# Kernel tuning notes

Hardware: AMD Instinct MI355X
Metric: run time of the kernel (lower is better)

The kernel has to match this reference:

```python
import jax, jax.numpy as jnp
import numpy as np

N_NODES = 100000
N_EDGES = 800000
HID = 128
LN_EPS = 1e-5


def _mlp2(x, w1, b1, w2, b2):
    # Linear -> ReLU -> Linear
    return jax.nn.relu(x @ w1 + b1) @ w2 + b2


def setup_inputs() -> dict:
    key = jax.random.key(0)
    ks = jax.random.split(key, 12)
    s = 1.0 / np.sqrt(3 * HID)
    s2 = 1.0 / np.sqrt(HID)
    return {
        "h": jax.random.normal(ks[0], (N_NODES, HID), dtype=jnp.float32),
        "edge_index": jax.random.randint(ks[1], (2, N_EDGES), 0, N_NODES, dtype=jnp.int64),
        "edge_x": jax.random.normal(ks[2], (N_EDGES, HID), dtype=jnp.float32),
        # edge_proj MLP (weights stored [in, out])
        "ep_w1": jax.random.uniform(ks[3], (3 * HID, HID), jnp.float32, -s, s),
        "ep_b1": jax.random.uniform(ks[4], (HID,), jnp.float32, -s, s),
        "ep_w2": jax.random.uniform(ks[5], (HID, HID), jnp.float32, -s2, s2),
        "ep_b2": jax.random.uniform(ks[6], (HID,), jnp.float32, -s2, s2),
        # update MLP
        "up_w1": jax.random.uniform(ks[7], (3 * HID, HID), jnp.float32, -s, s),
        "up_b1": jax.random.uniform(ks[8], (HID,), jnp.float32, -s, s),
        "up_w2": jax.random.uniform(ks[9], (HID, HID), jnp.float32, -s2, s2),
        "up_b2": jax.random.uniform(ks[10], (HID,), jnp.float32, -s2, s2),
        # LayerNorm affine
        "ln_g": jnp.ones((HID,), jnp.float32),
        "ln_b": jnp.zeros((HID,), jnp.float32),
    }


def reference(h, edge_index, edge_x, ep_w1, ep_b1, ep_w2, ep_b2,
              up_w1, up_b1, up_w2, up_b2, ln_g, ln_b):
    n = h.shape[0]
    src, dst = edge_index[0], edge_index[1]
    # edge gather + concat -> [E, 3H] -> message MLP -> [E, H]
    messages = _mlp2(jnp.concatenate([h[src], h[dst], edge_x], axis=-1),
                     ep_w1, ep_b1, ep_w2, ep_b2)
    # scatter-add aggregation for both directions
    incoming = jax.ops.segment_sum(messages, dst, num_segments=n)
    outgoing = jax.ops.segment_sum(messages, src, num_segments=n)
    # degree normalization (clamp min 1)
    ones = jnp.ones((edge_index.shape[1],), h.dtype)
    in_deg = jnp.maximum(jax.ops.segment_sum(ones, dst, num_segments=n), 1.0)[:, None]
    out_deg = jnp.maximum(jax.ops.segment_sum(ones, src, num_segments=n), 1.0)[:, None]
    updated = _mlp2(jnp.concatenate([h, incoming / in_deg, outgoing / out_deg], axis=-1),
                    up_w1, up_b1, up_w2, up_b2)
    # residual + LayerNorm
    x = h + updated
    mu = jnp.mean(x, axis=-1, keepdims=True)
    var = jnp.mean(jnp.square(x - mu), axis=-1, keepdims=True)
    return (x - mu) * jax.lax.rsqrt(var + LN_EPS) * ln_g + ln_b
```

## Files before the change

kernel.cpp:

```cpp
#include <hip/hip_runtime.h>
#include <stdint.h>

#define HIDD 128
#define NNODES 100000
#define NEDGES 800000

typedef short s16x8 __attribute__((ext_vector_type(8)));
typedef float f32x4 __attribute__((ext_vector_type(4)));

__device__ __forceinline__ short f2bf(float f) {
  union { float f; unsigned u; } v; v.f = f;
  return (short)((v.u + 0x7fffu + ((v.u >> 16) & 1u)) >> 16);
}
__device__ __forceinline__ short4 cvt4(float4 v) {
  short4 s; s.x = f2bf(v.x); s.y = f2bf(v.y); s.z = f2bf(v.z); s.w = f2bf(v.w);
  return s;
}
__device__ __forceinline__ float bflo(unsigned w) {
  union { unsigned u; float f; } v; v.u = w << 16; return v.f;
}
__device__ __forceinline__ float bfhi(unsigned w) {
  union { unsigned u; float f; } v; v.u = w & 0xffff0000u; return v.f;
}
__device__ __forceinline__ unsigned pack2(float a, float b) {
  return ((unsigned)(unsigned short)f2bf(b) << 16) | (unsigned)(unsigned short)f2bf(a);
}
__device__ __forceinline__ f32x4 mfma16(s16x8 a, s16x8 b, f32x4 c) {
  return __builtin_amdgcn_mfma_f32_16x16x32_bf16(a, b, c, 0, 0, 0);
}
__device__ __forceinline__ void atomic_pk_bf16(unsigned short* addr, unsigned pk) {
  asm volatile("global_atomic_pk_add_bf16 %0, %1, off" :: "v"(addr), "v"(pk) : "memory");
}

__global__ void k_prep_h(const float4* __restrict__ h4, short4* __restrict__ hb4, int n4) {
  int stride = gridDim.x * blockDim.x;
  for (int i = blockIdx.x * blockDim.x + threadIdx.x; i < n4; i += stride)
    hb4[i] = cvt4(h4[i]);
}

__global__ void k_prep_w(const float* __restrict__ w1e, const float* __restrict__ w2e,
                         const float* __restrict__ w1u, const float* __restrict__ w2u,
                         short* __restrict__ w1et, short* __restrict__ w2et,
                         short* __restrict__ w1ut, short* __restrict__ w2ut) {
  int i = blockIdx.x * 256 + threadIdx.x;
  if (i < 49152) {
    int n = i / 384, k = i - n * 384;
    w1et[i] = f2bf(w1e[k * 128 + n]);
    w1ut[i] = f2bf(w1u[k * 128 + n]);
  } else {
    int j = i - 49152;
    if (j < 16384) {
      int n = j >> 7, k = j & 127;
      int oc = (n & ~31) + 2 * (n & 15) + ((n >> 4) & 1);
      w2et[j] = f2bf(w2e[k * 128 + oc]);
      w2ut[j] = f2bf(w2u[k * 128 + n]);
    }
  }
}

__global__ __launch_bounds__(256, 2)
void k_edge(const short* __restrict__ hb, const int* __restrict__ eidx,
            const float* __restrict__ ex,
            const short* __restrict__ w1t, const short* __restrict__ w2t,
            const float* __restrict__ b1g, const float* __restrict__ b2g,
            unsigned short* __restrict__ incb, unsigned short* __restrict__ outgb,
            float* __restrict__ indeg, float* __restrict__ outdeg) {
  __shared__ __align__(16) short Xs[64][392];
  __shared__ __align__(16) short Hs[64][136];

  const int tid = threadIdx.x;
  const int wave = tid >> 6, lane = tid & 63;
  const int lg = lane >> 4, lr = lane & 15;
  const int koff = lg * 8;
  const int c0 = wave * 32 + lr, c1 = c0 + 16;
  const int pc0 = wave * 32 + 2 * lr;

  s16x8 wb1a[12], wb1b[12], wb2a[4], wb2b[4];
#pragma unroll
  for (int kk = 0; kk < 12; ++kk) {
    wb1a[kk] = *(const s16x8*)(w1t + c0 * 384 + kk * 32 + koff);
    wb1b[kk] = *(const s16x8*)(w1t + c1 * 384 + kk * 32 + koff);
  }
#pragma unroll
  for (int kk = 0; kk < 4; ++kk) {
    wb2a[kk] = *(const s16x8*)(w2t + c0 * 128 + kk * 32 + koff);
    wb2b[kk] = *(const s16x8*)(w2t + c1 * 128 + kk * 32 + koff);
  }
  const float bias1_0 = b1g[c0], bias1_1 = b1g[c1];
  const float bias2_0 = b2g[pc0], bias2_1 = b2g[pc0 + 1];

  for (int t = blockIdx.x; t < NEDGES / 64; t += gridDim.x) {
    const int base = t * 64;

    for (int u = tid; u < 64 * 32; u += 256) {
      int r = u >> 5, c = u & 31;
      int node = (c < 16) ? eidx[base + r] : eidx[NEDGES + base + r];
      *(int4*)&Xs[r][c * 8] = *(const int4*)(hb + (long)node * 128 + (c & 15) * 8);
    }
    for (int u = tid; u < 64 * 32; u += 256) {
      int r = u >> 5, q = u & 31;
      float4 v = *(const float4*)(ex + (long)(base + r) * 128 + q * 4);
      *(short4*)&Xs[r][256 + q * 4] = cvt4(v);
    }
    if (tid < 64) {
      atomicAdd(&outdeg[eidx[base + tid]], 1.0f);
      atomicAdd(&indeg[eidx[NEDGES + base + tid]], 1.0f);
    }
    __syncthreads();

    f32x4 acc[4][2] = {};
#pragma unroll
    for (int kk = 0; kk < 12; ++kk) {
      int k0 = kk * 32 + koff;
#pragma unroll
      for (int m = 0; m < 4; ++m) {
        s16x8 a = *(const s16x8*)&Xs[m * 16 + lr][k0];
        acc[m][0] = mfma16(a, wb1a[kk], acc[m][0]);
        acc[m][1] = mfma16(a, wb1b[kk], acc[m][1]);
      }
    }
#pragma unroll
    for (int m = 0; m < 4; ++m)
#pragma unroll
      for (int r2 = 0; r2 < 4; ++r2) {
        int row = m * 16 + lg * 4 + r2;
        Hs[row][c0] = f2bf(fmaxf(acc[m][0][r2] + bias1_0, 0.f));
        Hs[row][c1] = f2bf(fmaxf(acc[m][1][r2] + bias1_1, 0.f));
      }
    __syncthreads();

    f32x4 acc2[4][2] = {};
#pragma unroll
    for (int kk = 0; kk < 4; ++kk) {
      int k0 = kk * 32 + koff;
#pragma unroll
      for (int m = 0; m < 4; ++m) {
        s16x8 a = *(const s16x8*)&Hs[m * 16 + lr][k0];
        acc2[m][0] = mfma16(a, wb2a[kk], acc2[m][0]);
        acc2[m][1] = mfma16(a, wb2b[kk], acc2[m][1]);
      }
    }
#pragma unroll
    for (int m = 0; m < 4; ++m)
#pragma unroll
      for (int r2 = 0; r2 < 4; ++r2) {
        int row = m * 16 + lg * 4 + r2;
        int s = eidx[base + row], d = eidx[NEDGES + base + row];
        unsigned pk = pack2(acc2[m][0][r2] + bias2_0, acc2[m][1][r2] + bias2_1);
        atomic_pk_bf16(outgb + (long)s * 128 + pc0, pk);
        atomic_pk_bf16(incb + (long)d * 128 + pc0, pk);
      }
  }
}

__global__ __launch_bounds__(256, 2)
void k_node(const float* __restrict__ h, const short* __restrict__ hb,
            const unsigned short* __restrict__ incb,
            const unsigned short* __restrict__ outgb,
            const float* __restrict__ indeg, const float* __restrict__ outdeg,
            const short* __restrict__ w1t, const short* __restrict__ w2t,
            const float* __restrict__ b1g, const float* __restrict__ b2g,
            const float* __restrict__ lng, const float* __restrict__ lnb,
            float* __restrict__ out) {
  __shared__ __align__(16) char smem[67584];
  short (*Xs)[392] = (short (*)[392])smem;
  float (*Xf)[132] = (float (*)[132])smem;
  short (*Hs)[136] = (short (*)[136])(smem + 50176);

  const int tid = threadIdx.x;
  const int wave = tid >> 6, lane = tid & 63;
  const int lg = lane >> 4, lr = lane & 15;
  const int koff = lg * 8;
  const int c0 = wave * 32 + lr, c1 = c0 + 16;

  s16x8 wb1a[12], wb1b[12], wb2a[4], wb2b[4];
#pragma unroll
  for (int kk = 0; kk < 12; ++kk) {
    wb1a[kk] = *(const s16x8*)(w1t + c0 * 384 + kk * 32 + koff);
    wb1b[kk] = *(const s16x8*)(w1t + c1 * 384 + kk * 32 + koff);
  }
#pragma unroll
  for (int kk = 0; kk < 4; ++kk) {
    wb2a[kk] = *(const s16x8*)(w2t + c0 * 128 + kk * 32 + koff);
    wb2b[kk] = *(const s16x8*)(w2t + c1 * 128 + kk * 32 + koff);
  }
  const float bias1_0 = b1g[c0], bias1_1 = b1g[c1];
  const float bias2_0 = b2g[c0], bias2_1 = b2g[c1];

  const int ntiles = (NNODES + 63) / 64;
  for (int t = blockIdx.x; t < ntiles; t += gridDim.x) {
    const int base = t * 64;

    for (int u = tid; u < 64 * 16; u += 256) {
      int r = u >> 4, c = u & 15;
      long node = min(base + r, NNODES - 1);
      *(int4*)&Xs[r][c * 8] = *(const int4*)(hb + node * 128 + c * 8);
    }
    for (int u = tid; u < 64 * 16; u += 256) {
      int r = u >> 4, c = u & 15;
      long node = min(base + r, NNODES - 1);
      float s = 1.f / fmaxf(indeg[node], 1.f);
      uint4 w = *(const uint4*)(incb + node * 128 + c * 8);
      unsigned o0 = pack2(bflo(w.x) * s, bfhi(w.x) * s);
      unsigned o1 = pack2(bflo(w.y) * s, bfhi(w.y) * s);
      unsigned o2 = pack2(bflo(w.z) * s, bfhi(w.z) * s);
      unsigned o3 = pack2(bflo(w.w) * s, bfhi(w.w) * s);
      *(uint4*)&Xs[r][128 + c * 8] = make_uint4(o0, o1, o2, o3);
    }
    for (int u = tid; u < 64 * 16; u += 256) {
      int r = u >> 4, c = u & 15;
      long node = min(base + r, NNODES - 1);
      float s = 1.f / fmaxf(outdeg[node], 1.f);
      uint4 w = *(const uint4*)(outgb + node * 128 + c * 8);
      unsigned o0 = pack2(bflo(w.x) * s, bfhi(w.x) * s);
      unsigned o1 = pack2(bflo(w.y) * s, bfhi(w.y) * s);
      unsigned o2 = pack2(bflo(w.z) * s, bfhi(w.z) * s);
      unsigned o3 = pack2(bflo(w.w) * s, bfhi(w.w) * s);
      *(uint4*)&Xs[r][256 + c * 8] = make_uint4(o0, o1, o2, o3);
    }
    __syncthreads();

    f32x4 acc[4][2] = {};
#pragma unroll
    for (int kk = 0; kk < 12; ++kk) {
      int k0 = kk * 32 + koff;
#pragma unroll
      for (int m = 0; m < 4; ++m) {
        s16x8 a = *(const s16x8*)&Xs[m * 16 + lr][k0];
        acc[m][0] = mfma16(a, wb1a[kk], acc[m][0]);
        acc[m][1] = mfma16(a, wb1b[kk], acc[m][1]);
      }
    }
#pragma unroll
    for (int m = 0; m < 4; ++m)
#pragma unroll
      for (int r2 = 0; r2 < 4; ++r2) {
        int row = m * 16 + lg * 4 + r2;
        Hs[row][c0] = f2bf(fmaxf(acc[m][0][r2] + bias1_0, 0.f));
        Hs[row][c1] = f2bf(fmaxf(acc[m][1][r2] + bias1_1, 0.f));
      }
    __syncthreads();

    f32x4 acc2[4][2] = {};
#pragma unroll
    for (int kk = 0; kk < 4; ++kk) {
      int k0 = kk * 32 + koff;
#pragma unroll
      for (int m = 0; m < 4; ++m) {
        s16x8 a = *(const s16x8*)&Hs[m * 16 + lr][k0];
        acc2[m][0] = mfma16(a, wb2a[kk], acc2[m][0]);
        acc2[m][1] = mfma16(a, wb2b[kk], acc2[m][1]);
      }
    }
#pragma unroll
    for (int m = 0; m < 4; ++m)
#pragma unroll
      for (int r2 = 0; r2 < 4; ++r2) {
        int row = m * 16 + lg * 4 + r2;
        long node = base + row;
        float h0 = 0.f, h1 = 0.f;
        if (node < NNODES) { h0 = h[node * 128 + c0]; h1 = h[node * 128 + c1]; }
        Xf[row][c0] = acc2[m][0][r2] + bias2_0 + h0;
        Xf[row][c1] = acc2[m][1][r2] + bias2_1 + h1;
      }
    __syncthreads();

    {
      int r = tid >> 2, q = tid & 3;
      float sum = 0.f, ss = 0.f;
      float4 vals[8];
#pragma unroll
      for (int j = 0; j < 8; ++j) {
        float4 v = *(const float4*)&Xf[r][q * 32 + j * 4];
        vals[j] = v;
        sum += v.x + v.y + v.z + v.w;
        ss += v.x * v.x + v.y * v.y + v.z * v.z + v.w * v.w;
      }
      sum += __shfl_xor(sum, 1); sum += __shfl_xor(sum, 2);
      ss  += __shfl_xor(ss, 1);  ss  += __shfl_xor(ss, 2);
      float mean = sum * (1.f / 128.f);
      float var = ss * (1.f / 128.f) - mean * mean;
      float rstd = rsqrtf(var + 1e-5f);
      long node = base + r;
      if (node < NNODES) {
#pragma unroll
        for (int j = 0; j < 8; ++j) {
          int cc = q * 32 + j * 4;
          float4 v = vals[j];
          float4 o;
          o.x = (v.x - mean) * rstd * lng[cc + 0] + lnb[cc + 0];
          o.y = (v.y - mean) * rstd * lng[cc + 1] + lnb[cc + 1];
          o.z = (v.z - mean) * rstd * lng[cc + 2] + lnb[cc + 2];
          o.w = (v.w - mean) * rstd * lng[cc + 3] + lnb[cc + 3];
          *(float4*)(out + node * 128 + cc) = o;
        }
      }
    }
    __syncthreads();
  }
}

extern "C" void kernel_launch(void* const* d_in, const int* in_sizes, int n_in,
                              void* d_out, int out_size, void* d_ws, size_t ws_size,
                              hipStream_t stream) {
  const float* h    = (const float*)d_in[0];
  const int*   ei   = (const int*)d_in[1];
  const float* ex   = (const float*)d_in[2];
  const float* epw1 = (const float*)d_in[3];
  const float* epb1 = (const float*)d_in[4];
  const float* epw2 = (const float*)d_in[5];
  const float* epb2 = (const float*)d_in[6];
  const float* upw1 = (const float*)d_in[7];
  const float* upb1 = (const float*)d_in[8];
  const float* upw2 = (const float*)d_in[9];
  const float* upb2 = (const float*)d_in[10];
  const float* lng  = (const float*)d_in[11];
  const float* lnb  = (const float*)d_in[12];
  float* out = (float*)d_out;

  char* ws = (char*)d_ws;
  unsigned short* incb  = (unsigned short*)(ws);
  unsigned short* outgb = (unsigned short*)(ws + 25600000);
  float* indeg  = (float*)(ws + 51200000);
  float* outdeg = (float*)(ws + 51600000);
  short* hb     = (short*)(ws + 52000000);
  short* w1et   = (short*)(ws + 77600000);
  short* w2et   = (short*)(ws + 77698304);
  short* w1ut   = (short*)(ws + 77731072);
  short* w2ut   = (short*)(ws + 77829376);

  hipMemsetAsync(ws, 0, 52000000, stream);
  hipLaunchKernelGGL(k_prep_h, dim3(2048), dim3(256), 0, stream,
                     (const float4*)h, (short4*)hb, NNODES * 128 / 4);
  hipLaunchKernelGGL(k_prep_w, dim3(256), dim3(256), 0, stream,
                     epw1, epw2, upw1, upw2, w1et, w2et, w1ut, w2ut);
  hipLaunchKernelGGL(k_edge, dim3(1024), dim3(256), 0, stream,
                     hb, ei, ex, w1et, w2et, epb1, epb2, incb, outgb, indeg, outdeg);
  hipLaunchKernelGGL(k_node, dim3(512), dim3(256), 0, stream,
                     h, hb, incb, outgb, indeg, outdeg, w1ut, w2ut, upb1, upb2,
                     lng, lnb, out);
}
```

Measured before the change: 681.7 us.

## Load gathered node rows directly into MFMA operands, shrink LDS, raise occupancy

```diff
diff --git a/kernel.cpp b/kernel.cpp
--- a/kernel.cpp
+++ b/kernel.cpp
@@ -58,15 +58,15 @@
   }
 }
 
-__global__ __launch_bounds__(256, 2)
+__global__ __launch_bounds__(256, 3)
 void k_edge(const short* __restrict__ hb, const int* __restrict__ eidx,
             const float* __restrict__ ex,
             const short* __restrict__ w1t, const short* __restrict__ w2t,
             const float* __restrict__ b1g, const float* __restrict__ b2g,
             unsigned short* __restrict__ incb, unsigned short* __restrict__ outgb,
             float* __restrict__ indeg, float* __restrict__ outdeg) {
-  __shared__ __align__(16) short Xs[64][392];
-  __shared__ __align__(16) short Hs[64][136];
+  __shared__ __align__(16) short Xe[64][140];
+  __shared__ __align__(16) short Hs[64][140];
 
   const int tid = threadIdx.x;
   const int wave = tid >> 6, lane = tid & 63;
@@ -75,48 +75,72 @@
   const int c0 = wave * 32 + lr, c1 = c0 + 16;
   const int pc0 = wave * 32 + 2 * lr;
 
-  s16x8 wb1a[12], wb1b[12], wb2a[4], wb2b[4];
+  s16x8 wb1a[12], wb1b[12];
 #pragma unroll
   for (int kk = 0; kk < 12; ++kk) {
     wb1a[kk] = *(const s16x8*)(w1t + c0 * 384 + kk * 32 + koff);
     wb1b[kk] = *(const s16x8*)(w1t + c1 * 384 + kk * 32 + koff);
   }
-#pragma unroll
-  for (int kk = 0; kk < 4; ++kk) {
-    wb2a[kk] = *(const s16x8*)(w2t + c0 * 128 + kk * 32 + koff);
-    wb2b[kk] = *(const s16x8*)(w2t + c1 * 128 + kk * 32 + koff);
-  }
   const float bias1_0 = b1g[c0], bias1_1 = b1g[c1];
   const float bias2_0 = b2g[pc0], bias2_1 = b2g[pc0 + 1];
 
   for (int t = blockIdx.x; t < NEDGES / 64; t += gridDim.x) {
     const int base = t * 64;
 
-    for (int u = tid; u < 64 * 32; u += 256) {
-      int r = u >> 5, c = u & 31;
-      int node = (c < 16) ? eidx[base + r] : eidx[NEDGES + base + r];
-      *(int4*)&Xs[r][c * 8] = *(const int4*)(hb + (long)node * 128 + (c & 15) * 8);
-    }
-    for (int u = tid; u < 64 * 32; u += 256) {
-      int r = u >> 5, q = u & 31;
-      float4 v = *(const float4*)(ex + (long)(base + r) * 128 + q * 4);
-      *(short4*)&Xs[r][256 + q * 4] = cvt4(v);
+    for (int u = tid; u < 64 * 16; u += 256) {
+      int r = u >> 4, c = u & 15;
+      const float* p = ex + (long)(base + r) * 128 + c * 8;
+      float4 v0 = *(const float4*)p;
+      float4 v1 = *(const float4*)(p + 4);
+      short4 s0 = cvt4(v0), s1 = cvt4(v1);
+      *(int4*)&Xe[r][c * 8] = make_int4(
+        (int)(unsigned short)s0.x | ((int)(unsigned short)s0.y << 16),
+        (int)(unsigned short)s0.z | ((int)(unsigned short)s0.w << 16),
+        (int)(unsigned short)s1.x | ((int)(unsigned short)s1.y << 16),
+        (int)(unsigned short)s1.z | ((int)(unsigned short)s1.w << 16));
     }
     if (tid < 64) {
       atomicAdd(&outdeg[eidx[base + tid]], 1.0f);
       atomicAdd(&indeg[eidx[NEDGES + base + tid]], 1.0f);
     }
+    int sn[4], dn[4];
+#pragma unroll
+    for (int m = 0; m < 4; ++m) {
+      sn[m] = eidx[base + m * 16 + lr];
+      dn[m] = eidx[NEDGES + base + m * 16 + lr];
+    }
     __syncthreads();
 
     f32x4 acc[4][2] = {};
 #pragma unroll
-    for (int kk = 0; kk < 12; ++kk) {
-      int k0 = kk * 32 + koff;
-#pragma unroll
-      for (int m = 0; m < 4; ++m) {
-        s16x8 a = *(const s16x8*)&Xs[m * 16 + lr][k0];
-        acc[m][0] = mfma16(a, wb1a[kk], acc[m][0]);
-        acc[m][1] = mfma16(a, wb1b[kk], acc[m][1]);
+    for (int m = 0; m < 4; ++m) {
+      const short* ps = hb + (long)sn[m] * 128 + koff;
+      {
+        s16x8 a0 = *(const s16x8*)(ps);
+        s16x8 a1 = *(const s16x8*)(ps + 32);
+        s16x8 a2 = *(const s16x8*)(ps + 64);
+        s16x8 a3 = *(const s16x8*)(ps + 96);
+        acc[m][0] = mfma16(a0, wb1a[0], acc[m][0]); acc[m][1] = mfma16(a0, wb1b[0], acc[m][1]);
+        acc[m][0] = mfma16(a1, wb1a[1], acc[m][0]); acc[m][1] = mfma16(a1, wb1b[1], acc[m][1]);
+        acc[m][0] = mfma16(a2, wb1a[2], acc[m][0]); acc[m][1] = mfma16(a2, wb1b[2], acc[m][1]);
+        acc[m][0] = mfma16(a3, wb1a[3], acc[m][0]); acc[m][1] = mfma16(a3, wb1b[3], acc[m][1]);
+      }
+      const short* pd = hb + (long)dn[m] * 128 + koff;
+      {
+        s16x8 a0 = *(const s16x8*)(pd);
+        s16x8 a1 = *(const s16x8*)(pd + 32);
+        s16x8 a2 = *(const s16x8*)(pd + 64);
+        s16x8 a3 = *(const s16x8*)(pd + 96);
+        acc[m][0] = mfma16(a0, wb1a[4], acc[m][0]); acc[m][1] = mfma16(a0, wb1b[4], acc[m][1]);
+        acc[m][0] = mfma16(a1, wb1a[5], acc[m][0]); acc[m][1] = mfma16(a1, wb1b[5], acc[m][1]);
+        acc[m][0] = mfma16(a2, wb1a[6], acc[m][0]); acc[m][1] = mfma16(a2, wb1b[6], acc[m][1]);
+        acc[m][0] = mfma16(a3, wb1a[7], acc[m][0]); acc[m][1] = mfma16(a3, wb1b[7], acc[m][1]);
+      }
+#pragma unroll
+      for (int kk = 0; kk < 4; ++kk) {
+        s16x8 a = *(const s16x8*)&Xe[m * 16 + lr][kk * 32 + koff];
+        acc[m][0] = mfma16(a, wb1a[8 + kk], acc[m][0]);
+        acc[m][1] = mfma16(a, wb1b[8 + kk], acc[m][1]);
       }
     }
 #pragma unroll
@@ -132,12 +156,13 @@
     f32x4 acc2[4][2] = {};
 #pragma unroll
     for (int kk = 0; kk < 4; ++kk) {
-      int k0 = kk * 32 + koff;
+      s16x8 w2a = *(const s16x8*)(w2t + c0 * 128 + kk * 32 + koff);
+      s16x8 w2b = *(const s16x8*)(w2t + c1 * 128 + kk * 32 + koff);
 #pragma unroll
       for (int m = 0; m < 4; ++m) {
-        s16x8 a = *(const s16x8*)&Hs[m * 16 + lr][k0];
-        acc2[m][0] = mfma16(a, wb2a[kk], acc2[m][0]);
-        acc2[m][1] = mfma16(a, wb2b[kk], acc2[m][1]);
+        s16x8 a = *(const s16x8*)&Hs[m * 16 + lr][kk * 32 + koff];
+        acc2[m][0] = mfma16(a, w2a, acc2[m][0]);
+        acc2[m][1] = mfma16(a, w2b, acc2[m][1]);
       }
     }
 #pragma unroll
@@ -334,7 +359,7 @@
                      (const float4*)h, (short4*)hb, NNODES * 128 / 4);
   hipLaunchKernelGGL(k_prep_w, dim3(256), dim3(256), 0, stream,
                      epw1, epw2, upw1, upw2, w1et, w2et, w1ut, w2ut);
-  hipLaunchKernelGGL(k_edge, dim3(1024), dim3(256), 0, stream,
+  hipLaunchKernelGGL(k_edge, dim3(2048), dim3(256), 0, stream,
                      hb, ei, ex, w1et, w2et, epb1, epb2, incb, outgb, indeg, outdeg);
   hipLaunchKernelGGL(k_node, dim3(512), dim3(256), 0, stream,
                      h, hb, incb, outgb, indeg, outdeg, w1ut, w2ut, upb1, upb2,
```

After: 910.9 us. 1.34x slower.

## Load edge features directly into MFMA registers, shrinking LDS and raising occupancy

Applied to the files above, without the earlier changes.

```diff
diff --git a/kernel.cpp b/kernel.cpp
--- a/kernel.cpp
+++ b/kernel.cpp
@@ -24,6 +24,13 @@
 }
 __device__ __forceinline__ unsigned pack2(float a, float b) {
   return ((unsigned)(unsigned short)f2bf(b) << 16) | (unsigned)(unsigned short)f2bf(a);
+}
+__device__ __forceinline__ s16x8 cvt8(const float* p) {
+  float4 v0 = *(const float4*)p, v1 = *(const float4*)(p + 4);
+  union { s16x8 s; uint4 u; } r;
+  r.u = make_uint4(pack2(v0.x, v0.y), pack2(v0.z, v0.w),
+                   pack2(v1.x, v1.y), pack2(v1.z, v1.w));
+  return r.s;
 }
 __device__ __forceinline__ f32x4 mfma16(s16x8 a, s16x8 b, f32x4 c) {
   return __builtin_amdgcn_mfma_f32_16x16x32_bf16(a, b, c, 0, 0, 0);
@@ -58,14 +65,14 @@
   }
 }
 
-__global__ __launch_bounds__(256, 2)
+__global__ __launch_bounds__(256, 3)
 void k_edge(const short* __restrict__ hb, const int* __restrict__ eidx,
             const float* __restrict__ ex,
             const short* __restrict__ w1t, const short* __restrict__ w2t,
             const float* __restrict__ b1g, const float* __restrict__ b2g,
             unsigned short* __restrict__ incb, unsigned short* __restrict__ outgb,
             float* __restrict__ indeg, float* __restrict__ outdeg) {
-  __shared__ __align__(16) short Xs[64][392];
+  __shared__ __align__(16) short Xs[64][264];
   __shared__ __align__(16) short Hs[64][136];
 
   const int tid = threadIdx.x;
@@ -97,11 +104,6 @@
       int node = (c < 16) ? eidx[base + r] : eidx[NEDGES + base + r];
       *(int4*)&Xs[r][c * 8] = *(const int4*)(hb + (long)node * 128 + (c & 15) * 8);
     }
-    for (int u = tid; u < 64 * 32; u += 256) {
-      int r = u >> 5, q = u & 31;
-      float4 v = *(const float4*)(ex + (long)(base + r) * 128 + q * 4);
-      *(short4*)&Xs[r][256 + q * 4] = cvt4(v);
-    }
     if (tid < 64) {
       atomicAdd(&outdeg[eidx[base + tid]], 1.0f);
       atomicAdd(&indeg[eidx[NEDGES + base + tid]], 1.0f);
@@ -110,13 +112,26 @@
 
     f32x4 acc[4][2] = {};
 #pragma unroll
-    for (int kk = 0; kk < 12; ++kk) {
-      int k0 = kk * 32 + koff;
-#pragma unroll
-      for (int m = 0; m < 4; ++m) {
-        s16x8 a = *(const s16x8*)&Xs[m * 16 + lr][k0];
+    for (int m = 0; m < 4; ++m) {
+      const int row = m * 16 + lr;
+      const float* pe = ex + (long)(base + row) * 128 + koff;
+#pragma unroll
+      for (int kk = 0; kk < 4; ++kk) {
+        s16x8 a = *(const s16x8*)&Xs[row][kk * 32 + koff];
         acc[m][0] = mfma16(a, wb1a[kk], acc[m][0]);
         acc[m][1] = mfma16(a, wb1b[kk], acc[m][1]);
+      }
+#pragma unroll
+      for (int kk = 0; kk < 4; ++kk) {
+        s16x8 a = *(const s16x8*)&Xs[row][128 + kk * 32 + koff];
+        acc[m][0] = mfma16(a, wb1a[4 + kk], acc[m][0]);
+        acc[m][1] = mfma16(a, wb1b[4 + kk], acc[m][1]);
+      }
+#pragma unroll
+      for (int kk = 0; kk < 4; ++kk) {
+        s16x8 a = cvt8(pe + kk * 32);
+        acc[m][0] = mfma16(a, wb1a[8 + kk], acc[m][0]);
+        acc[m][1] = mfma16(a, wb1b[8 + kk], acc[m][1]);
       }
     }
 #pragma unroll
@@ -132,10 +147,9 @@
     f32x4 acc2[4][2] = {};
 #pragma unroll
     for (int kk = 0; kk < 4; ++kk) {
-      int k0 = kk * 32 + koff;
 #pragma unroll
       for (int m = 0; m < 4; ++m) {
-        s16x8 a = *(const s16x8*)&Hs[m * 16 + lr][k0];
+        s16x8 a = *(const s16x8*)&Hs[m * 16 + lr][kk * 32 + koff];
         acc2[m][0] = mfma16(a, wb2a[kk], acc2[m][0]);
         acc2[m][1] = mfma16(a, wb2b[kk], acc2[m][1]);
       }
@@ -334,7 +348,7 @@
                      (const float4*)h, (short4*)hb, NNODES * 128 / 4);
   hipLaunchKernelGGL(k_prep_w, dim3(256), dim3(256), 0, stream,
                      epw1, epw2, upw1, upw2, w1et, w2et, w1ut, w2ut);
-  hipLaunchKernelGGL(k_edge, dim3(1024), dim3(256), 0, stream,
+  hipLaunchKernelGGL(k_edge, dim3(768), dim3(256), 0, stream,
                      hb, ei, ex, w1et, w2et, epb1, epb2, incb, outgb, indeg, outdeg);
   hipLaunchKernelGGL(k_node, dim3(512), dim3(256), 0, stream,
                      h, hb, incb, outgb, indeg, outdeg, w1ut, w2ut, upb1, upb2,
```

New measurement: 1.017 ms. 49.2% more time.

## Replace atomic scatter-add with CSR-sorted gather aggregation of per-edge messages

Applied to the files above, without the earlier changes.

```diff
diff --git a/kernel.cpp b/kernel.cpp
--- a/kernel.cpp
+++ b/kernel.cpp
@@ -4,6 +4,7 @@
 #define HIDD 128
 #define NNODES 100000
 #define NEDGES 800000
+#define NSEG 196
 
 typedef short s16x8 __attribute__((ext_vector_type(8)));
 typedef float f32x4 __attribute__((ext_vector_type(4)));
@@ -58,13 +59,88 @@
   }
 }
 
+__global__ void k_hist(const int* __restrict__ eidx, int* __restrict__ cnt_s,
+                       int* __restrict__ cnt_d) {
+  int i = blockIdx.x * 256 + threadIdx.x;
+  if (i < NEDGES) {
+    atomicAdd(&cnt_s[eidx[i]], 1);
+    atomicAdd(&cnt_d[eidx[NEDGES + i]], 1);
+  }
+}
+
+__global__ void k_bsum(const int* __restrict__ cnt_d, const int* __restrict__ cnt_s,
+                       int* __restrict__ bsum) {
+  __shared__ int red[256];
+  int gb = blockIdx.x, sel = gb >= NSEG, b = gb - sel * NSEG;
+  const int* cnt = sel ? cnt_s : cnt_d;
+  int t = threadIdx.x;
+  int i0 = b * 512 + 2 * t;
+  int a = (i0 < NNODES) ? cnt[i0] : 0;
+  int c = (i0 + 1 < NNODES) ? cnt[i0 + 1] : 0;
+  red[t] = a + c;
+  __syncthreads();
+  for (int d = 128; d > 0; d >>= 1) {
+    if (t < d) red[t] += red[t + d];
+    __syncthreads();
+  }
+  if (t == 0) bsum[gb] = red[0];
+}
+
+__global__ void k_soff(int* __restrict__ bsum, int* __restrict__ off_d,
+                       int* __restrict__ off_s) {
+  if (threadIdx.x == 0) {
+    int tot = 0;
+    for (int i = 0; i < NSEG; ++i) { int v = bsum[i]; bsum[i] = tot; tot += v; }
+    off_d[NNODES] = tot;
+  } else if (threadIdx.x == 1) {
+    int tot = 0;
+    for (int i = NSEG; i < 2 * NSEG; ++i) { int v = bsum[i]; bsum[i] = tot; tot += v; }
+    off_s[NNODES] = tot;
+  }
+}
+
+__global__ void k_sfin(const int* __restrict__ cnt_d, const int* __restrict__ cnt_s,
+                       const int* __restrict__ bsum,
+                       int* __restrict__ off_d, int* __restrict__ off_s,
+                       int* __restrict__ cur_d, int* __restrict__ cur_s) {
+  __shared__ int p[256];
+  int gb = blockIdx.x, sel = gb >= NSEG, b = gb - sel * NSEG;
+  const int* cnt = sel ? cnt_s : cnt_d;
+  int* off = sel ? off_s : off_d;
+  int* cur = sel ? cur_s : cur_d;
+  int t = threadIdx.x;
+  int i0 = b * 512 + 2 * t;
+  int a = (i0 < NNODES) ? cnt[i0] : 0;
+  int c = (i0 + 1 < NNODES) ? cnt[i0 + 1] : 0;
+  p[t] = a + c;
+  __syncthreads();
+  for (int d = 1; d < 256; d <<= 1) {
+    int v = (t >= d) ? p[t - d] : 0;
+    __syncthreads();
+    p[t] += v;
+    __syncthreads();
+  }
+  int excl = (t ? p[t - 1] : 0) + bsum[gb];
+  if (i0 < NNODES)     { off[i0] = excl;     cur[i0] = excl; }
+  if (i0 + 1 < NNODES) { off[i0 + 1] = excl + a; cur[i0 + 1] = excl + a; }
+}
+
+__global__ void k_scat(const int* __restrict__ eidx, int* __restrict__ cur_s,
+                       int* __restrict__ cur_d, int* __restrict__ slist,
+                       int* __restrict__ dlist) {
+  int i = blockIdx.x * 256 + threadIdx.x;
+  if (i < NEDGES) {
+    slist[atomicAdd(&cur_s[eidx[i]], 1)] = i;
+    dlist[atomicAdd(&cur_d[eidx[NEDGES + i]], 1)] = i;
+  }
+}
+
 __global__ __launch_bounds__(256, 2)
-void k_edge(const short* __restrict__ hb, const int* __restrict__ eidx,
-            const float* __restrict__ ex,
-            const short* __restrict__ w1t, const short* __restrict__ w2t,
-            const float* __restrict__ b1g, const float* __restrict__ b2g,
-            unsigned short* __restrict__ incb, unsigned short* __restrict__ outgb,
-            float* __restrict__ indeg, float* __restrict__ outdeg) {
+void k_edge2(const short* __restrict__ hb, const int* __restrict__ eidx,
+             const float* __restrict__ ex,
+             const short* __restrict__ w1t, const short* __restrict__ w2t,
+             const float* __restrict__ b1g, const float* __restrict__ b2g,
+             unsigned* __restrict__ msgd) {
   __shared__ __align__(16) short Xs[64][392];
   __shared__ __align__(16) short Hs[64][136];
 
@@ -102,10 +178,6 @@
       float4 v = *(const float4*)(ex + (long)(base + r) * 128 + q * 4);
       *(short4*)&Xs[r][256 + q * 4] = cvt4(v);
     }
-    if (tid < 64) {
-      atomicAdd(&outdeg[eidx[base + tid]], 1.0f);
-      atomicAdd(&indeg[eidx[NEDGES + base + tid]], 1.0f);
-    }
     __syncthreads();
 
     f32x4 acc[4][2] = {};
@@ -132,10 +204,9 @@
     f32x4 acc2[4][2] = {};
 #pragma unroll
     for (int kk = 0; kk < 4; ++kk) {
-      int k0 = kk * 32 + koff;
-#pragma unroll
-      for (int m = 0; m < 4; ++m) {
-        s16x8 a = *(const s16x8*)&Hs[m * 16 + lr][k0];
+#pragma unroll
+      for (int m = 0; m < 4; ++m) {
+        s16x8 a = *(const s16x8*)&Hs[m * 16 + lr][kk * 32 + koff];
         acc2[m][0] = mfma16(a, wb2a[kk], acc2[m][0]);
         acc2[m][1] = mfma16(a, wb2b[kk], acc2[m][1]);
       }
@@ -145,23 +216,21 @@
 #pragma unroll
       for (int r2 = 0; r2 < 4; ++r2) {
         int row = m * 16 + lg * 4 + r2;
-        int s = eidx[base + row], d = eidx[NEDGES + base + row];
-        unsigned pk = pack2(acc2[m][0][r2] + bias2_0, acc2[m][1][r2] + bias2_1);
-        atomic_pk_bf16(outgb + (long)s * 128 + pc0, pk);
-        atomic_pk_bf16(incb + (long)d * 128 + pc0, pk);
+        msgd[(long)(base + row) * 64 + wave * 16 + lr] =
+            pack2(acc2[m][0][r2] + bias2_0, acc2[m][1][r2] + bias2_1);
       }
   }
 }
 
 __global__ __launch_bounds__(256, 2)
-void k_node(const float* __restrict__ h, const short* __restrict__ hb,
-            const unsigned short* __restrict__ incb,
-            const unsigned short* __restrict__ outgb,
-            const float* __restrict__ indeg, const float* __restrict__ outdeg,
-            const short* __restrict__ w1t, const short* __restrict__ w2t,
-            const float* __restrict__ b1g, const float* __restrict__ b2g,
-            const float* __restrict__ lng, const float* __restrict__ lnb,
-            float* __restrict__ out) {
+void k_node2(const float* __restrict__ h, const short* __restrict__ hb,
+             const unsigned short* __restrict__ msg,
+             const int* __restrict__ off_d, const int* __restrict__ dlist,
+             const int* __restrict__ off_s, const int* __restrict__ slist,
+             const short* __restrict__ w1t, const short* __restrict__ w2t,
+             const float* __restrict__ b1g, const float* __restrict__ b2g,
+             const float* __restrict__ lng, const float* __restrict__ lnb,
+             float* __restrict__ out) {
   __shared__ __align__(16) char smem[67584];
   short (*Xs)[392] = (short (*)[392])smem;
   float (*Xf)[132] = (float (*)[132])smem;
@@ -196,30 +265,279 @@
       long node = min(base + r, NNODES - 1);
       *(int4*)&Xs[r][c * 8] = *(const int4*)(hb + node * 128 + c * 8);
     }
+    {
+      int r = tid >> 2, q = tid & 3;
+      long node = base + r;
+      bool valid = node < NNODES;
+#pragma unroll
+      for (int dir = 0; dir < 2; ++dir) {
+        const int* off = dir ? off_s : off_d;
+        const int* lst = dir ? slist : dlist;
+        float av[32];
+#pragma unroll
+        for (int j = 0; j < 32; ++j) av[j] = 0.f;
+        int e0 = 0, e1 = 0;
+        if (valid) { e0 = off[node]; e1 = off[node + 1]; }
+        for (int e = e0; e < e1; ++e) {
+          int eid = lst[e];
+          const uint4* mp = (const uint4*)(msg + (long)eid * 128 + q * 32);
+          uint4 u0 = mp[0], u1 = mp[1], u2 = mp[2], u3 = mp[3];
+          av[0]  += bflo(u0.x); av[1]  += bfhi(u0.x);
+          av[2]  += bflo(u0.y); av[3]  += bfhi(u0.y);
+          av[4]  += bflo(u0.z); av[5]  += bfhi(u0.z);
+          av[6]  += bflo(u0.w); av[7]  += bfhi(u0.w);
+          av[8]  += bflo(u1.x); av[9]  += bfhi(u1.x);
+          av[10] += bflo(u1.y); av[11] += bfhi(u1.y);
+          av[12] += bflo(u1.z); av[13] += bfhi(u1.z);
+          av[14] += bflo(u1.w); av[15] += bfhi(u1.w);
+          av[16] += bflo(u2.x); av[17] += bfhi(u2.x);
+          av[18] += bflo(u2.y); av[19] += bfhi(u2.y);
+          av[20] += bflo(u2.z); av[21] += bfhi(u2.z);
+          av[22] += bflo(u2.w); av[23] += bfhi(u2.w);
+          av[24] += bflo(u3.x); av[25] += bfhi(u3.x);
+          av[26] += bflo(u3.y); av[27] += bfhi(u3.y);
+          av[28] += bflo(u3.z); av[29] += bfhi(u3.z);
+          av[30] += bflo(u3.w); av[31] += bfhi(u3.w);
+        }
+        float sc = 1.f / fmaxf((float)(e1 - e0), 1.f);
+        unsigned pk[16];
+#pragma unroll
+        for (int j = 0; j < 16; ++j) pk[j] = pack2(av[2 * j] * sc, av[2 * j + 1] * sc);
+        uint4* dst = (uint4*)&Xs[r][(dir ? 256 : 128) + q * 32];
+        dst[0] = make_uint4(pk[0], pk[1], pk[2], pk[3]);
+        dst[1] = make_uint4(pk[4], pk[5], pk[6], pk[7]);
+        dst[2] = make_uint4(pk[8], pk[9], pk[10], pk[11]);
+        dst[3] = make_uint4(pk[12], pk[13], pk[14], pk[15]);
+      }
+    }
+    __syncthreads();
+
+    f32x4 acc[4][2] = {};
+#pragma unroll
+    for (int kk = 0; kk < 12; ++kk) {
+      int k0 = kk * 32 + koff;
+#pragma unroll
+      for (int m = 0; m < 4; ++m) {
+        s16x8 a = *(const s16x8*)&Xs[m * 16 + lr][k0];
+        acc[m][0] = mfma16(a, wb1a[kk], acc[m][0]);
+        acc[m][1] = mfma16(a, wb1b[kk], acc[m][1]);
+      }
+    }
+#pragma unroll
+    for (int m = 0; m < 4; ++m)
+#pragma unroll
+      for (int r2 = 0; r2 < 4; ++r2) {
+        int row = m * 16 + lg * 4 + r2;
+        Hs[row][c0] = f2bf(fmaxf(acc[m][0][r2] + bias1_0, 0.f));
+        Hs[row][c1] = f2bf(fmaxf(acc[m][1][r2] + bias1_1, 0.f));
+      }
+    __syncthreads();
+
+    f32x4 acc2[4][2] = {};
+#pragma unroll
+    for (int kk = 0; kk < 4; ++kk) {
+      int k0 = kk * 32 + koff;
+#pragma unroll
+      for (int m = 0; m < 4; ++m) {
+        s16x8 a = *(const s16x8*)&Hs[m * 16 + lr][k0];
+        acc2[m][0] = mfma16(a, wb2a[kk], acc2[m][0]);
+        acc2[m][1] = mfma16(a, wb2b[kk], acc2[m][1]);
+      }
+    }
+#pragma unroll
+    for (int m = 0; m < 4; ++m)
+#pragma unroll
+      for (int r2 = 0; r2 < 4; ++r2) {
+        int row = m * 16 + lg * 4 + r2;
+        long node = base + row;
+        float h0 = 0.f, h1 = 0.f;
+        if (node < NNODES) { h0 = h[node * 128 + c0]; h1 = h[node * 128 + c1]; }
+        Xf[row][c0] = acc2[m][0][r2] + bias2_0 + h0;
+        Xf[row][c1] = acc2[m][1][r2] + bias2_1 + h1;
+      }
+    __syncthreads();
+
+    {
+      int r = tid >> 2, q = tid & 3;
+      float sum = 0.f, ss = 0.f;
+      float4 vals[8];
+#pragma unroll
+      for (int j = 0; j < 8; ++j) {
+        float4 v = *(const float4*)&Xf[r][q * 32 + j * 4];
+        vals[j] = v;
+        sum += v.x + v.y + v.z + v.w;
+        ss += v.x * v.x + v.y * v.y + v.z * v.z + v.w * v.w;
+      }
+      sum += __shfl_xor(sum, 1); sum += __shfl_xor(sum, 2);
+      ss  += __shfl_xor(ss, 1);  ss  += __shfl_xor(ss, 2);
+      float mean = sum * (1.f / 128.f);
+      float var = ss * (1.f / 128.f) - mean * mean;
+      float rstd = rsqrtf(var + 1e-5f);
+      long node = base + r;
+      if (node < NNODES) {
+#pragma unroll
+        for (int j = 0; j < 8; ++j) {
+          int cc = q * 32 + j * 4;
+          float4 v = vals[j];
+          float4 o;
+          o.x = (v.x - mean) * rstd * lng[cc + 0] + lnb[cc + 0];
+          o.y = (v.y - mean) * rstd * lng[cc + 1] + lnb[cc + 1];
+          o.z = (v.z - mean) * rstd * lng[cc + 2] + lnb[cc + 2];
+          o.w = (v.w - mean) * rstd * lng[cc + 3] + lnb[cc + 3];
+          *(float4*)(out + node * 128 + cc) = o;
+        }
+      }
+    }
+    __syncthreads();
+  }
+}
+
+__global__ __launch_bounds__(256, 2)
+void k_edge_at(const short* __restrict__ hb, const int* __restrict__ eidx,
+               const float* __restrict__ ex,
+               const short* __restrict__ w1t, const short* __restrict__ w2t,
+               const float* __restrict__ b1g, const float* __restrict__ b2g,
+               unsigned short* __restrict__ incb, unsigned short* __restrict__ outgb,
+               float* __restrict__ indeg, float* __restrict__ outdeg) {
+  __shared__ __align__(16) short Xs[64][392];
+  __shared__ __align__(16) short Hs[64][136];
+  const int tid = threadIdx.x;
+  const int wave = tid >> 6, lane = tid & 63;
+  const int lg = lane >> 4, lr = lane & 15;
+  const int koff = lg * 8;
+  const int c0 = wave * 32 + lr, c1 = c0 + 16;
+  const int pc0 = wave * 32 + 2 * lr;
+  s16x8 wb1a[12], wb1b[12], wb2a[4], wb2b[4];
+#pragma unroll
+  for (int kk = 0; kk < 12; ++kk) {
+    wb1a[kk] = *(const s16x8*)(w1t + c0 * 384 + kk * 32 + koff);
+    wb1b[kk] = *(const s16x8*)(w1t + c1 * 384 + kk * 32 + koff);
+  }
+#pragma unroll
+  for (int kk = 0; kk < 4; ++kk) {
+    wb2a[kk] = *(const s16x8*)(w2t + c0 * 128 + kk * 32 + koff);
+    wb2b[kk] = *(const s16x8*)(w2t + c1 * 128 + kk * 32 + koff);
+  }
+  const float bias1_0 = b1g[c0], bias1_1 = b1g[c1];
+  const float bias2_0 = b2g[pc0], bias2_1 = b2g[pc0 + 1];
+  for (int t = blockIdx.x; t < NEDGES / 64; t += gridDim.x) {
+    const int base = t * 64;
+    for (int u = tid; u < 64 * 32; u += 256) {
+      int r = u >> 5, c = u & 31;
+      int node = (c < 16) ? eidx[base + r] : eidx[NEDGES + base + r];
+      *(int4*)&Xs[r][c * 8] = *(const int4*)(hb + (long)node * 128 + (c & 15) * 8);
+    }
+    for (int u = tid; u < 64 * 32; u += 256) {
+      int r = u >> 5, q = u & 31;
+      float4 v = *(const float4*)(ex + (long)(base + r) * 128 + q * 4);
+      *(short4*)&Xs[r][256 + q * 4] = cvt4(v);
+    }
+    if (tid < 64) {
+      atomicAdd(&outdeg[eidx[base + tid]], 1.0f);
+      atomicAdd(&indeg[eidx[NEDGES + base + tid]], 1.0f);
+    }
+    __syncthreads();
+    f32x4 acc[4][2] = {};
+#pragma unroll
+    for (int kk = 0; kk < 12; ++kk) {
+      int k0 = kk * 32 + koff;
+#pragma unroll
+      for (int m = 0; m < 4; ++m) {
+        s16x8 a = *(const s16x8*)&Xs[m * 16 + lr][k0];
+        acc[m][0] = mfma16(a, wb1a[kk], acc[m][0]);
+        acc[m][1] = mfma16(a, wb1b[kk], acc[m][1]);
+      }
+    }
+#pragma unroll
+    for (int m = 0; m < 4; ++m)
+#pragma unroll
+      for (int r2 = 0; r2 < 4; ++r2) {
+        int row = m * 16 + lg * 4 + r2;
+        Hs[row][c0] = f2bf(fmaxf(acc[m][0][r2] + bias1_0, 0.f));
+        Hs[row][c1] = f2bf(fmaxf(acc[m][1][r2] + bias1_1, 0.f));
+      }
+    __syncthreads();
+    f32x4 acc2[4][2] = {};
+#pragma unroll
+    for (int kk = 0; kk < 4; ++kk) {
+#pragma unroll
+      for (int m = 0; m < 4; ++m) {
+        s16x8 a = *(const s16x8*)&Hs[m * 16 + lr][kk * 32 + koff];
+        acc2[m][0] = mfma16(a, wb2a[kk], acc2[m][0]);
+        acc2[m][1] = mfma16(a, wb2b[kk], acc2[m][1]);
+      }
+    }
+#pragma unroll
+    for (int m = 0; m < 4; ++m)
+#pragma unroll
+      for (int r2 = 0; r2 < 4; ++r2) {
+        int row = m * 16 + lg * 4 + r2;
+        int s = eidx[base + row], d = eidx[NEDGES + base + row];
+        unsigned pk = pack2(acc2[m][0][r2] + bias2_0, acc2[m][1][r2] + bias2_1);
+        atomic_pk_bf16(outgb + (long)s * 128 + pc0, pk);
+        atomic_pk_bf16(incb + (long)d * 128 + pc0, pk);
+      }
+  }
+}
+
+__global__ __launch_bounds__(256, 2)
+void k_node_at(const float* __restrict__ h, const short* __restrict__ hb,
+               const unsigned short* __restrict__ incb,
+               const unsigned short* __restrict__ outgb,
+               const float* __restrict__ indeg, const float* __restrict__ outdeg,
+               const short* __restrict__ w1t, const short* __restrict__ w2t,
+               const float* __restrict__ b1g, const float* __restrict__ b2g,
+               const float* __restrict__ lng, const float* __restrict__ lnb,
+               float* __restrict__ out) {
+  __shared__ __align__(16) char smem[67584];
+  short (*Xs)[392] = (short (*)[392])smem;
+  float (*Xf)[132] = (float (*)[132])smem;
+  short (*Hs)[136] = (short (*)[136])(smem + 50176);
+  const int tid = threadIdx.x;
+  const int wave = tid >> 6, lane = tid & 63;
+  const int lg = lane >> 4, lr = lane & 15;
+  const int koff = lg * 8;
+  const int c0 = wave * 32 + lr, c1 = c0 + 16;
+  s16x8 wb1a[12], wb1b[12], wb2a[4], wb2b[4];
+#pragma unroll
+  for (int kk = 0; kk < 12; ++kk) {
+    wb1a[kk] = *(const s16x8*)(w1t + c0 * 384 + kk * 32 + koff);
+    wb1b[kk] = *(const s16x8*)(w1t + c1 * 384 + kk * 32 + koff);
+  }
+#pragma unroll
+  for (int kk = 0; kk < 4; ++kk) {
+    wb2a[kk] = *(const s16x8*)(w2t + c0 * 128 + kk * 32 + koff);
+    wb2b[kk] = *(const s16x8*)(w2t + c1 * 128 + kk * 32 + koff);
+  }
+  const float bias1_0 = b1g[c0], bias1_1 = b1g[c1];
+  const float bias2_0 = b2g[c0], bias2_1 = b2g[c1];
+  const int ntiles = (NNODES + 63) / 64;
+  for (int t = blockIdx.x; t < ntiles; t += gridDim.x) {
+    const int base = t * 64;
+    for (int u = tid; u < 64 * 16; u += 256) {
+      int r = u >> 4, c = u & 15;
+      long node = min(base + r, NNODES - 1);
+      *(int4*)&Xs[r][c * 8] = *(const int4*)(hb + node * 128 + c * 8);
+    }
     for (int u = tid; u < 64 * 16; u += 256) {
       int r = u >> 4, c = u & 15;
       long node = min(base + r, NNODES - 1);
       float s = 1.f / fmaxf(indeg[node], 1.f);
       uint4 w = *(const uint4*)(incb + node * 128 + c * 8);
-      unsigned o0 = pack2(bflo(w.x) * s, bfhi(w.x) * s);
-      unsigned o1 = pack2(bflo(w.y) * s, bfhi(w.y) * s);
-      unsigned o2 = pack2(bflo(w.z) * s, bfhi(w.z) * s);
-      unsigned o3 = pack2(bflo(w.w) * s, bfhi(w.w) * s);
-      *(uint4*)&Xs[r][128 + c * 8] = make_uint4(o0, o1, o2, o3);
+      *(uint4*)&Xs[r][128 + c * 8] = make_uint4(
+        pack2(bflo(w.x) * s, bfhi(w.x) * s), pack2(bflo(w.y) * s, bfhi(w.y) * s),
+        pack2(bflo(w.z) * s, bfhi(w.z) * s), pack2(bflo(w.w) * s, bfhi(w.w) * s));
     }
     for (int u = tid; u < 64 * 16; u += 256) {
       int r = u >> 4, c = u & 15;
       long node = min(base + r, NNODES - 1);
       float s = 1.f / fmaxf(outdeg[node], 1.f);
       uint4 w = *(const uint4*)(outgb + node * 128 + c * 8);
-      unsigned o0 = pack2(bflo(w.x) * s, bfhi(w.x) * s);
-      unsigned o1 = pack2(bflo(w.y) * s, bfhi(w.y) * s);
-      unsigned o2 = pack2(bflo(w.z) * s, bfhi(w.z) * s);
-      unsigned o3 = pack2(bflo(w.w) * s, bfhi(w.w) * s);
-      *(uint4*)&Xs[r][256 + c * 8] = make_uint4(o0, o1, o2, o3);
-    }
-    __syncthreads();
-
+      *(uint4*)&Xs[r][256 + c * 8] = make_uint4(
+        pack2(bflo(w.x) * s, bfhi(w.x) * s), pack2(bflo(w.y) * s, bfhi(w.y) * s),
+        pack2(bflo(w.z) * s, bfhi(w.z) * s), pack2(bflo(w.w) * s, bfhi(w.w) * s));
+    }
+    __syncthreads();
     f32x4 acc[4][2] = {};
 #pragma unroll
     for (int kk = 0; kk < 12; ++kk) {
@@ -240,7 +558,6 @@
         Hs[row][c1] = f2bf(fmaxf(acc[m][1][r2] + bias1_1, 0.f));
       }
     __syncthreads();
-
     f32x4 acc2[4][2] = {};
 #pragma unroll
     for (int kk = 0; kk < 4; ++kk) {
@@ -264,7 +581,6 @@
         Xf[row][c1] = acc2[m][1][r2] + bias2_1 + h1;
       }
     __syncthreads();
-
     {
       int r = tid >> 2, q = tid & 3;
       float sum = 0.f, ss = 0.f;
@@ -317,26 +633,65 @@
   const float* lng  = (const float*)d_in[11];
   const float* lnb  = (const float*)d_in[12];
   float* out = (float*)d_out;
-
   char* ws = (char*)d_ws;
-  unsigned short* incb  = (unsigned short*)(ws);
-  unsigned short* outgb = (unsigned short*)(ws + 25600000);
-  float* indeg  = (float*)(ws + 51200000);
-  float* outdeg = (float*)(ws + 51600000);
-  short* hb     = (short*)(ws + 52000000);
-  short* w1et   = (short*)(ws + 77600000);
-  short* w2et   = (short*)(ws + 77698304);
-  short* w1ut   = (short*)(ws + 77731072);
-  short* w2ut   = (short*)(ws + 77829376);
-
-  hipMemsetAsync(ws, 0, 52000000, stream);
-  hipLaunchKernelGGL(k_prep_h, dim3(2048), dim3(256), 0, stream,
-                     (const float4*)h, (short4*)hb, NNODES * 128 / 4);
-  hipLaunchKernelGGL(k_prep_w, dim3(256), dim3(256), 0, stream,
-                     epw1, epw2, upw1, upw2, w1et, w2et, w1ut, w2ut);
-  hipLaunchKernelGGL(k_edge, dim3(1024), dim3(256), 0, stream,
-                     hb, ei, ex, w1et, w2et, epb1, epb2, incb, outgb, indeg, outdeg);
-  hipLaunchKernelGGL(k_node, dim3(512), dim3(256), 0, stream,
-                     h, hb, incb, outgb, indeg, outdeg, w1ut, w2ut, upb1, upb2,
-                     lng, lnb, out);
-}
+
+  const size_t NEED = 239500000;
+  if (ws_size >= NEED) {
+    unsigned short* msg = (unsigned short*)(ws);
+    short* hb    = (short*)(ws + 204800000);
+    short* w1et  = (short*)(ws + 230400000);
+    short* w2et  = (short*)(ws + 230498304);
+    short* w1ut  = (short*)(ws + 230531072);
+    short* w2ut  = (short*)(ws + 230629376);
+    int* cnt_d   = (int*)(ws + 230662144);
+    int* cnt_s   = (int*)(ws + 231062144);
+    int* off_d   = (int*)(ws + 231462144);
+    int* off_s   = (int*)(ws + 231862148);
+    int* cur_d   = (int*)(ws + 232262152);
+    int* cur_s   = (int*)(ws + 232662152);
+    int* dlist   = (int*)(ws + 233062152);
+    int* slist   = (int*)(ws + 236262152);
+    int* bsum    = (int*)(ws + 239462152);
+
+    hipMemsetAsync(cnt_d, 0, 800000, stream);
+    hipLaunchKernelGGL(k_prep_h, dim3(2048), dim3(256), 0, stream,
+                       (const float4*)h, (short4*)hb, NNODES * 128 / 4);
+    hipLaunchKernelGGL(k_prep_w, dim3(256), dim3(256), 0, stream,
+                       epw1, epw2, upw1, upw2, w1et, w2et, w1ut, w2ut);
+    hipLaunchKernelGGL(k_hist, dim3((NEDGES + 255) / 256), dim3(256), 0, stream,
+                       ei, cnt_s, cnt_d);
+    hipLaunchKernelGGL(k_bsum, dim3(2 * NSEG), dim3(256), 0, stream,
+                       cnt_d, cnt_s, bsum);
+    hipLaunchKernelGGL(k_soff, dim3(1), dim3(64), 0, stream, bsum, off_d, off_s);
+    hipLaunchKernelGGL(k_sfin, dim3(2 * NSEG), dim3(256), 0, stream,
+                       cnt_d, cnt_s, bsum, off_d, off_s, cur_d, cur_s);
+    hipLaunchKernelGGL(k_scat, dim3((NEDGES + 255) / 256), dim3(256), 0, stream,
+                       ei, cur_s, cur_d, slist, dlist);
+    hipLaunchKernelGGL(k_edge2, dim3(1024), dim3(256), 0, stream,
+                       hb, ei, ex, w1et, w2et, epb1, epb2, (unsigned*)msg);
+    hipLaunchKernelGGL(k_node2, dim3(512), dim3(256), 0, stream,
+                       h, hb, msg, off_d, dlist, off_s, slist,
+                       w1ut, w2ut, upb1, upb2, lng, lnb, out);
+  } else {
+    unsigned short* incb  = (unsigned short*)(ws);
+    unsigned short* outgb = (unsigned short*)(ws + 25600000);
+    float* indeg  = (float*)(ws + 51200000);
+    float* outdeg = (float*)(ws + 51600000);
+    short* hb     = (short*)(ws + 52000000);
+    short* w1et   = (short*)(ws + 77600000);
+    short* w2et   = (short*)(ws + 77698304);
+    short* w1ut   = (short*)(ws + 77731072);
+    short* w2ut   = (short*)(ws + 77829376);
+
+    hipMemsetAsync(ws, 0, 52000000, stream);
+    hipLaunchKernelGGL(k_prep_h, dim3(2048), dim3(256), 0, stream,
+                       (const float4*)h, (short4*)hb, NNODES * 128 / 4);
+    hipLaunchKernelGGL(k_prep_w, dim3(256), dim3(256), 0, stream,
+                       epw1, epw2, upw1, upw2, w1et, w2et, w1ut, w2ut);
+    hipLaunchKernelGGL(k_edge_at, dim3(1024), dim3(256), 0, stream,
+                       hb, ei, ex, w1et, w2et, epb1, epb2, incb, outgb, indeg, outdeg);
+    hipLaunchKernelGGL(k_node_at, dim3(512), dim3(256), 0, stream,
+                       h, hb, incb, outgb, indeg, outdeg, w1ut, w2ut, upb1, upb2,
+                       lng, lnb, out);
+  }
+}
```

Result: slower. 756.3 us (+10.9%).
